# Kernel optimization log

Measured on AMD Instinct MI355X. Metric: run time of the kernel, lower is better.

## Reference

```python
import jax, jax.numpy as jnp
import numpy as np

B, I, H = 8192, 1024, 1024

def setup_inputs() -> dict:
    key = jax.random.key(0)
    ks = jax.random.split(key, 6)
    s_in = 1.0 / np.sqrt(I)
    s_h = 1.0 / np.sqrt(H)
    return {
        "x": jax.random.normal(ks[0], (B, I), jnp.float32),
        "h_prev": jax.random.normal(ks[1], (B, H), jnp.float32),
        "c_prev": jax.random.normal(ks[2], (B, H), jnp.float32),
        "Wx": jax.random.normal(ks[3], (4, H, I), jnp.float32) * s_in,   # gate order: input, forget, cell, output
        "Wh": jax.random.normal(ks[4], (4, H, H), jnp.float32) * s_h,
        "bh": jax.random.normal(ks[5], (4, H), jnp.float32) * s_h,
    }

def reference(x, h_prev, c_prev, Wx, Wh, bh):
    # Fused: 2 batched GEMMs for all 4 gates -> [B, 4, H]
    gates = (jnp.einsum('bi,ghi->bgh', x, Wx)
             + jnp.einsum('bk,ghk->bgh', h_prev, Wh)
             + bh[None, :, :])
    i = jax.nn.sigmoid(gates[:, 0])
    f = jax.nn.sigmoid(gates[:, 1])
    g = jnp.tanh(gates[:, 2])
    o = jax.nn.sigmoid(gates[:, 3])
    c_next = f * c_prev + i * g
    h_next = o * jnp.tanh(c_next)
    return (h_next, c_next)
```

## Files before the change

### kernel.cpp

```cpp
#include <hip/hip_runtime.h>
#include <hip/hip_bf16.h>
#include <stdint.h>

#define B_DIM 8192
#define I_DIM 1024
#define H_DIM 1024
#define KTOT  2048
#define NTILES 32

typedef __attribute__((ext_vector_type(8))) short short8;
typedef __attribute__((ext_vector_type(4))) float f32x4;

static __device__ __forceinline__ short f2b(float f) {
    __bf16 h = (__bf16)f;
    return __builtin_bit_cast(short, h);
}

static __device__ __forceinline__ short8 pack8(float4 a, float4 b) {
    short8 s;
    s[0] = f2b(a.x); s[1] = f2b(a.y); s[2] = f2b(a.z); s[3] = f2b(a.w);
    s[4] = f2b(b.x); s[5] = f2b(b.y); s[6] = f2b(b.z); s[7] = f2b(b.w);
    return s;
}

static __device__ __forceinline__ float sigmoid_f(float x) {
    return 1.0f / (1.0f + __expf(-x));
}

static __device__ __forceinline__ float tanh_fast(float x) {
    x = fminf(fmaxf(x, -15.0f), 15.0f);
    float e = __expf(2.0f * x);
    return (e - 1.0f) / (e + 1.0f);
}

static __device__ __forceinline__ void load_lds16(const void* gptr, void* lptr) {
    __builtin_amdgcn_global_load_lds(
        (const __attribute__((address_space(1))) uint32_t*)gptr,
        (__attribute__((address_space(3))) uint32_t*)lptr, 16, 0, 0);
}

__global__ __launch_bounds__(256) void convert_kernel(
    const float* __restrict__ x, const float* __restrict__ h,
    const float* __restrict__ wx, const float* __restrict__ wh,
    short* __restrict__ Aw, short* __restrict__ Bw)
{
    const int64_t nx = (int64_t)B_DIM * I_DIM / 8;
    const int64_t nw = (int64_t)4 * H_DIM * I_DIM / 8;
    const int64_t total = 2 * nx + 2 * nw;
    for (int64_t g = (int64_t)blockIdx.x * blockDim.x + threadIdx.x; g < total;
         g += (int64_t)gridDim.x * blockDim.x) {
        const float* src;
        short* dst;
        if (g < nx) {
            int64_t r = g >> 7, kc = (g & 127) * 8;
            src = x + g * 8; dst = Aw + r * 2048 + kc;
        } else if (g < 2 * nx) {
            int64_t gg = g - nx;
            int64_t r = gg >> 7, kc = (gg & 127) * 8;
            src = h + gg * 8; dst = Aw + r * 2048 + 1024 + kc;
        } else if (g < 2 * nx + nw) {
            int64_t gg = g - 2 * nx;
            int64_t r = gg >> 7, kc = (gg & 127) * 8;
            src = wx + gg * 8; dst = Bw + r * 2048 + kc;
        } else {
            int64_t gg = g - 2 * nx - nw;
            int64_t r = gg >> 7, kc = (gg & 127) * 8;
            src = wh + gg * 8; dst = Bw + r * 2048 + 1024 + kc;
        }
        float4 v0 = ((const float4*)src)[0];
        float4 v1 = ((const float4*)src)[1];
        *(short8*)dst = pack8(v0, v1);
    }
}


#define AOFF(d, kp, f) ((d) * 16384 + (kp) * 8192 + (f) * 512)
#define BOFF(d, kp, f) (32768 + (d) * 16384 + (kp) * 8192 + (f) * 512)

#define STAGE_A(dn, kh, tkp) \
    load_lds16(aSrc0 + (size_t)(tkp) * 64 + (kh) * 32, &smem[AOFF(dn, kh, 2 * w)]); \
    load_lds16(aSrc1 + (size_t)(tkp) * 64 + (kh) * 32, &smem[AOFF(dn, kh, 2 * w + 1)]);

#define STAGE_B(dn, kh, tkp) \
    load_lds16(bSrc0 + (size_t)(tkp) * 64 + (kh) * 32, &smem[BOFF(dn, kh, 2 * w)]); \
    load_lds16(bSrc1 + (size_t)(tkp) * 64 + (kh) * 32, &smem[BOFF(dn, kh, 2 * w + 1)]);

#define VM4 asm volatile("s_waitcnt vmcnt(4)" ::: "memory");

#define PH(d, kp, mh, AV, BV, STAGE_STMT, EXTRAWAIT) do { \
    _Pragma("unroll") \
    for (int j = 0; j < 4; ++j) \
        BV[j] = *(const short8*)&smem[BOFF(d, kp, wn * 4 + j) + lane * 8]; \
    _Pragma("unroll") \
    for (int i = 0; i < 4; ++i) \
        AV[i] = *(const short8*)&smem[AOFF(d, kp, wm * 8 + (mh) * 4 + i) + lane * 8]; \
    STAGE_STMT \
    __builtin_amdgcn_s_barrier(); \
    __builtin_amdgcn_s_setprio(1); \
    _Pragma("unroll") \
    for (int i = 0; i < 4; ++i) \
        _Pragma("unroll") \
        for (int j = 0; j < 4; ++j) \
            acc[(mh) * 4 + i][j] = __builtin_amdgcn_mfma_f32_16x16x32_bf16( \
                AV[i], BV[j], acc[(mh) * 4 + i][j], 0, 0, 0); \
    __builtin_amdgcn_s_setprio(0); \
    EXTRAWAIT \
    __builtin_amdgcn_s_barrier(); \
} while (0)

#define TILE(d, tn) do { \
    PH(d, 0, 0, avA, bvA, STAGE_A(d ^ 1, 0, tn), ); \
    PH(d, 0, 1, avB, bvB, STAGE_B(d ^ 1, 0, tn), VM4); \
    PH(d, 1, 0, avA, bvA, STAGE_A(d ^ 1, 1, tn), ); \
    PH(d, 1, 1, avB, bvB, STAGE_B(d ^ 1, 1, tn), VM4); \
} while (0)

__global__ __launch_bounds__(512, 2) void lstm_gemm8_kernel(
    const short* __restrict__ Aw, const short* __restrict__ Bw,
    const float* __restrict__ cprev, const float* __restrict__ bh,
    float* __restrict__ out)
{
    extern __shared__ __align__(16) short smem[];

    int bid = blockIdx.x;
    bid = (bid & 7) * 64 + (bid >> 3);
    const int bm = bid >> 4;
    const int bn = bid & 15;
    const int m0 = bm * 256;
    const int h0 = bn * 64;

    const int t    = threadIdx.x;
    const int lane = t & 63;
    const int w    = t >> 6;
    const int wm   = w >> 2;
    const int wn   = w & 3;
    const int lc   = lane & 15;
    const int lk   = lane >> 4;

    const short* aSrc0 = Aw + (size_t)(m0 + (2 * w + 0) * 16 + lc) * 2048 + lk * 8;
    const short* aSrc1 = Aw + (size_t)(m0 + (2 * w + 1) * 16 + lc) * 2048 + lk * 8;
    const int cf0 = 2 * w, cf1 = 2 * w + 1;
    const short* bSrc0 = Bw + (size_t)((cf0 & 3) * 1024 + h0 + ((cf0 >> 2) << 4) + lc) * 2048 + lk * 8;
    const short* bSrc1 = Bw + (size_t)((cf1 & 3) * 1024 + h0 + ((cf1 >> 2) << 4) + lc) * 2048 + lk * 8;

    f32x4 acc[8][4] = {};
    short8 avA[4], avB[4], bvA[4], bvB[4];

    STAGE_A(0, 0, 0)
    STAGE_B(0, 0, 0)
    STAGE_A(0, 1, 0)
    STAGE_B(0, 1, 0)
    asm volatile("s_waitcnt vmcnt(0)" ::: "memory");
    __builtin_amdgcn_s_barrier();

    #pragma unroll 1
    for (int tk2 = 0; tk2 < 16; ++tk2) {
        const int t1  = 2 * tk2 + 1;
        const int tp1 = (t1 + 1 < NTILES) ? t1 + 1 : t1;
        TILE(0, t1);
        TILE(1, tp1);
    }
    asm volatile("s_waitcnt vmcnt(0)" ::: "memory");

    const int rg = lane >> 4;
    const int h  = h0 + wn * 16 + lc;
    const float b_i = bh[0 * H_DIM + h];
    const float b_f = bh[1 * H_DIM + h];
    const float b_g = bh[2 * H_DIM + h];
    const float b_o = bh[3 * H_DIM + h];

    #pragma unroll
    for (int mf = 0; mf < 8; ++mf) {
        #pragma unroll
        for (int r = 0; r < 4; ++r) {
            const int row = m0 + wm * 128 + mf * 16 + rg * 4 + r;
            const float pi = acc[mf][0][r] + b_i;
            const float pf = acc[mf][1][r] + b_f;
            const float pg = acc[mf][2][r] + b_g;
            const float po = acc[mf][3][r] + b_o;
            const float iv = sigmoid_f(pi);
            const float fv = sigmoid_f(pf);
            const float gv = tanh_fast(pg);
            const float ov = sigmoid_f(po);
            const float cp = cprev[(size_t)row * H_DIM + h];
            const float cn = fv * cp + iv * gv;
            const float hn = ov * tanh_fast(cn);
            out[(size_t)row * H_DIM + h] = hn;
            out[(size_t)B_DIM * H_DIM + (size_t)row * H_DIM + h] = cn;
        }
    }
}

static __device__ __forceinline__ int swz(int row, int k) {
    int byte = (row << 7) + (k << 1);
    byte ^= (row & 7) << 4;
    return byte >> 1;
}

__global__ __launch_bounds__(256, 2) void lstm_fallback_kernel(
    const float* __restrict__ x, const float* __restrict__ hprev,
    const float* __restrict__ cprev, const float* __restrict__ Wx,
    const float* __restrict__ Wh, const float* __restrict__ bh,
    float* __restrict__ out)
{
    __shared__ __align__(16) short As[128 * 64];
    __shared__ __align__(16) short Bs[128 * 64];

    int bid = blockIdx.x;
    bid = (bid & 7) * 256 + (bid >> 3);
    const int mt = bid >> 5;
    const int ht = bid & 31;
    const int m0 = mt * 128;
    const int h0 = ht * 32;

    const int t    = threadIdx.x;
    const int lane = t & 63;
    const int w    = t >> 6;
    const int wr   = w >> 1;
    const int wc   = w & 1;

    const int srow = t >> 3;
    const int sk   = (t & 7) * 8;

    f32x4 acc[4][4] = {};

    #pragma unroll 1
    for (int phase = 0; phase < 2; ++phase) {
        const float* __restrict__ Ap = phase ? hprev : x;
        const float* __restrict__ Bp = phase ? Wh : Wx;
        #pragma unroll 1
        for (int kk = 0; kk < 1024; kk += 64) {
            __syncthreads();
            #pragma unroll
            for (int p = 0; p < 4; ++p) {
                const int row = srow + p * 32;
                const float4* src = (const float4*)(Ap + (size_t)(m0 + row) * I_DIM + kk + sk);
                *(short8*)&As[swz(row, sk)] = pack8(src[0], src[1]);
            }
            #pragma unroll
            for (int p = 0; p < 4; ++p) {
                const int n    = srow + p * 32;
                const int gate = (n >> 4) & 3;
                const int hcol = h0 + ((n >> 6) << 4) + (n & 15);
                const float4* src = (const float4*)(Bp + (size_t)((gate << 10) + hcol) * 1024 + kk + sk);
                *(short8*)&Bs[swz(n, sk)] = pack8(src[0], src[1]);
            }
            __syncthreads();
            #pragma unroll
            for (int ks = 0; ks < 2; ++ks) {
                const int kb = ks * 32 + ((lane >> 4) << 3);
                short8 a[4], b[4];
                #pragma unroll
                for (int m = 0; m < 4; ++m)
                    a[m] = *(const short8*)&As[swz(wr * 64 + m * 16 + (lane & 15), kb)];
                #pragma unroll
                for (int j = 0; j < 4; ++j)
                    b[j] = *(const short8*)&Bs[swz(wc * 64 + j * 16 + (lane & 15), kb)];
                #pragma unroll
                for (int m = 0; m < 4; ++m)
                    #pragma unroll
                    for (int j = 0; j < 4; ++j)
                        acc[m][j] = __builtin_amdgcn_mfma_f32_16x16x32_bf16(a[m], b[j], acc[m][j], 0, 0, 0);
            }
        }
    }

    const int cl = lane & 15;
    const int rg = lane >> 4;
    const int h  = h0 + wc * 16 + cl;
    const float b_i = bh[0 * H_DIM + h];
    const float b_f = bh[1 * H_DIM + h];
    const float b_g = bh[2 * H_DIM + h];
    const float b_o = bh[3 * H_DIM + h];

    #pragma unroll
    for (int m = 0; m < 4; ++m) {
        #pragma unroll
        for (int r = 0; r < 4; ++r) {
            const int row = m0 + wr * 64 + m * 16 + rg * 4 + r;
            const float pi = acc[m][0][r] + b_i;
            const float pf = acc[m][1][r] + b_f;
            const float pg = acc[m][2][r] + b_g;
            const float po = acc[m][3][r] + b_o;
            const float iv = sigmoid_f(pi);
            const float fv = sigmoid_f(pf);
            const float gv = tanh_fast(pg);
            const float ov = sigmoid_f(po);
            const float cp = cprev[(size_t)row * H_DIM + h];
            const float cn = fv * cp + iv * gv;
            const float hn = ov * tanh_fast(cn);
            out[(size_t)row * H_DIM + h] = hn;
            out[(size_t)B_DIM * H_DIM + (size_t)row * H_DIM + h] = cn;
        }
    }
}

extern "C" void kernel_launch(void* const* d_in, const int* in_sizes, int n_in,
                              void* d_out, int out_size, void* d_ws, size_t ws_size,
                              hipStream_t stream) {
    const float* x     = (const float*)d_in[0];
    const float* hprev = (const float*)d_in[1];
    const float* cprev = (const float*)d_in[2];
    const float* Wx    = (const float*)d_in[3];
    const float* Wh    = (const float*)d_in[4];
    const float* bh    = (const float*)d_in[5];
    float* out = (float*)d_out;

    const size_t need = ((size_t)B_DIM * 2048 + (size_t)4096 * 2048) * sizeof(short);
    if (ws_size >= need && d_ws != nullptr) {
        (void)hipFuncSetAttribute((const void*)lstm_gemm8_kernel,
                                  hipFuncAttributeMaxDynamicSharedMemorySize, 131072);
        short* Aw = (short*)d_ws;
        short* Bw = Aw + (size_t)B_DIM * 2048;
        hipLaunchKernelGGL(convert_kernel, dim3(2048), dim3(256), 0, stream,
                           x, hprev, Wx, Wh, Aw, Bw);
        hipLaunchKernelGGL(lstm_gemm8_kernel, dim3(512), dim3(512), 131072, stream,
                           Aw, Bw, cprev, bh, out);
    } else {
        hipLaunchKernelGGL(lstm_fallback_kernel, dim3(2048), dim3(256), 0, stream,
                           x, hprev, cprev, Wx, Wh, bh, out);
    }
}
```

Before: 174.7 us.

## Restructure K-tile schedule: one barrier per tile, all prefetches issued upfront

Each K-tile previously ran as four phases with two barriers apiece. It now has a single barrier per tile. All four global-to-LDS prefetches for the next tile are issued at the start, and LDS fragment reads are interleaved with the MFMA groups using an extra A register set. The aim is to cut barrier synchronization overhead and overlap LDS reads with matrix math. The trade-off is higher register pressure from the additional short8 fragments, plus a full vmcnt(0) wait at the end of each tile that may expose global load latency.

```diff
diff --git a/kernel.cpp b/kernel.cpp
--- a/kernel.cpp
+++ b/kernel.cpp
@@ -85,17 +85,17 @@
     load_lds16(bSrc0 + (size_t)(tkp) * 64 + (kh) * 32, &smem[BOFF(dn, kh, 2 * w)]); \
     load_lds16(bSrc1 + (size_t)(tkp) * 64 + (kh) * 32, &smem[BOFF(dn, kh, 2 * w + 1)]);
 
-#define VM4 asm volatile("s_waitcnt vmcnt(4)" ::: "memory");
-
-#define PH(d, kp, mh, AV, BV, STAGE_STMT, EXTRAWAIT) do { \
+#define RD_B(d, kp, BV) { \
     _Pragma("unroll") \
     for (int j = 0; j < 4; ++j) \
-        BV[j] = *(const short8*)&smem[BOFF(d, kp, wn * 4 + j) + lane * 8]; \
+        BV[j] = *(const short8*)&smem[BOFF(d, kp, wn * 4 + j) + lane * 8]; }
+
+#define RD_A(d, kp, mh, AV) { \
     _Pragma("unroll") \
     for (int i = 0; i < 4; ++i) \
-        AV[i] = *(const short8*)&smem[AOFF(d, kp, wm * 8 + (mh) * 4 + i) + lane * 8]; \
-    STAGE_STMT \
-    __builtin_amdgcn_s_barrier(); \
+        AV[i] = *(const short8*)&smem[AOFF(d, kp, wm * 8 + (mh) * 4 + i) + lane * 8]; }
+
+#define MFMA16(mh, AV, BV) { \
     __builtin_amdgcn_s_setprio(1); \
     _Pragma("unroll") \
     for (int i = 0; i < 4; ++i) \
@@ -103,16 +103,25 @@
         for (int j = 0; j < 4; ++j) \
             acc[(mh) * 4 + i][j] = __builtin_amdgcn_mfma_f32_16x16x32_bf16( \
                 AV[i], BV[j], acc[(mh) * 4 + i][j], 0, 0, 0); \
-    __builtin_amdgcn_s_setprio(0); \
-    EXTRAWAIT \
+    __builtin_amdgcn_s_setprio(0); }
+
+#define TILE(d, tn) do { \
+    RD_B(d, 0, bv0) \
+    RD_A(d, 0, 0, av0) \
+    STAGE_A(d ^ 1, 0, tn) \
+    STAGE_B(d ^ 1, 0, tn) \
+    STAGE_A(d ^ 1, 1, tn) \
+    STAGE_B(d ^ 1, 1, tn) \
+    RD_A(d, 0, 1, av1) \
+    MFMA16(0, av0, bv0) \
+    RD_B(d, 1, bv1) \
+    RD_A(d, 1, 0, av2) \
+    MFMA16(1, av1, bv0) \
+    RD_A(d, 1, 1, av0) \
+    MFMA16(0, av2, bv1) \
+    MFMA16(1, av0, bv1) \
+    asm volatile("s_waitcnt vmcnt(0)" ::: "memory"); \
     __builtin_amdgcn_s_barrier(); \
-} while (0)
-
-#define TILE(d, tn) do { \
-    PH(d, 0, 0, avA, bvA, STAGE_A(d ^ 1, 0, tn), ); \
-    PH(d, 0, 1, avB, bvB, STAGE_B(d ^ 1, 0, tn), VM4); \
-    PH(d, 1, 0, avA, bvA, STAGE_A(d ^ 1, 1, tn), ); \
-    PH(d, 1, 1, avB, bvB, STAGE_B(d ^ 1, 1, tn), VM4); \
 } while (0)
 
 __global__ __launch_bounds__(512, 2) void lstm_gemm8_kernel(
@@ -144,7 +153,7 @@
     const short* bSrc1 = Bw + (size_t)((cf1 & 3) * 1024 + h0 + ((cf1 >> 2) << 4) + lc) * 2048 + lk * 8;
 
     f32x4 acc[8][4] = {};
-    short8 avA[4], avB[4], bvA[4], bvB[4];
+    short8 av0[4], av1[4], av2[4], bv0[4], bv1[4];
 
     STAGE_A(0, 0, 0)
     STAGE_B(0, 0, 0)
```

After: 192.2 us. 1.1x slower.

## Pre-tile bf16 operands into MFMA fragment order for contiguous LDS staging

Applied to the files above, without the earlier changes.

The conversion kernel now writes A and B in a fragment-blocked layout: 16-row fragments by K-tile by half, with 64 lanes of 8 bf16 each. Each direct-to-LDS load of a wave therefore reads a contiguous 1 KB chunk instead of 16 rows strided by 4 KB. The weight fragments are also pre-permuted by gate and column block, which simplifies address math in the GEMM. In exchange, the conversion kernel now does strided, scattered reads from the fp32 sources, and its grid is doubled.

```diff
diff --git a/kernel.cpp b/kernel.cpp
--- a/kernel.cpp
+++ b/kernel.cpp
@@ -39,33 +39,45 @@
         (__attribute__((address_space(3))) uint32_t*)lptr, 16, 0, 0);
 }
 
+#define GA_GROUPS (512 * 32 * 2 * 64)
+#define GB_GROUPS (256 * 32 * 2 * 64)
+
 __global__ __launch_bounds__(256) void convert_kernel(
     const float* __restrict__ x, const float* __restrict__ h,
     const float* __restrict__ wx, const float* __restrict__ wh,
     short* __restrict__ Aw, short* __restrict__ Bw)
 {
-    const int64_t nx = (int64_t)B_DIM * I_DIM / 8;
-    const int64_t nw = (int64_t)4 * H_DIM * I_DIM / 8;
-    const int64_t total = 2 * nx + 2 * nw;
+    const int64_t total = (int64_t)GA_GROUPS + GB_GROUPS;
     for (int64_t g = (int64_t)blockIdx.x * blockDim.x + threadIdx.x; g < total;
          g += (int64_t)gridDim.x * blockDim.x) {
         const float* src;
         short* dst;
-        if (g < nx) {
-            int64_t r = g >> 7, kc = (g & 127) * 8;
-            src = x + g * 8; dst = Aw + r * 2048 + kc;
-        } else if (g < 2 * nx) {
-            int64_t gg = g - nx;
-            int64_t r = gg >> 7, kc = (gg & 127) * 8;
-            src = h + gg * 8; dst = Aw + r * 2048 + 1024 + kc;
-        } else if (g < 2 * nx + nw) {
-            int64_t gg = g - 2 * nx;
-            int64_t r = gg >> 7, kc = (gg & 127) * 8;
-            src = wx + gg * 8; dst = Bw + r * 2048 + kc;
+        if (g < GA_GROUPS) {
+            const int lane = (int)(g & 63);
+            const int rest = (int)(g >> 6);
+            const int kh   = rest & 1;
+            const int tk   = (rest >> 1) & 31;
+            const int mfrag = rest >> 6;
+            const int row = (mfrag << 4) + (lane & 15);
+            const int k   = (tk << 6) + (kh << 5) + ((lane >> 4) << 3);
+            src = (k < 1024) ? (x + (size_t)row * 1024 + k)
+                             : (h + (size_t)row * 1024 + (k - 1024));
+            dst = Aw + (size_t)g * 8;
         } else {
-            int64_t gg = g - 2 * nx - nw;
-            int64_t r = gg >> 7, kc = (gg & 127) * 8;
-            src = wh + gg * 8; dst = Bw + r * 2048 + 1024 + kc;
+            const int64_t gb = g - GA_GROUPS;
+            const int lane = (int)(gb & 63);
+            const int rest = (int)(gb >> 6);
+            const int kh   = rest & 1;
+            const int tk   = (rest >> 1) & 31;
+            const int nfrag = rest >> 6;
+            const int cf   = nfrag & 15;
+            const int bn   = nfrag >> 4;
+            const int gate = cf & 3;
+            const int col  = (bn << 6) + ((cf >> 2) << 4) + (lane & 15);
+            const int k    = (tk << 6) + (kh << 5) + ((lane >> 4) << 3);
+            src = (k < 1024) ? (wx + ((size_t)(gate << 10) + col) * 1024 + k)
+                             : (wh + ((size_t)(gate << 10) + col) * 1024 + (k - 1024));
+            dst = Bw + (size_t)gb * 8;
         }
         float4 v0 = ((const float4*)src)[0];
         float4 v1 = ((const float4*)src)[1];
@@ -78,12 +90,12 @@
 #define BOFF(d, kp, f) (32768 + (d) * 16384 + (kp) * 8192 + (f) * 512)
 
 #define STAGE_A(dn, kh, tkp) \
-    load_lds16(aSrc0 + (size_t)(tkp) * 64 + (kh) * 32, &smem[AOFF(dn, kh, 2 * w)]); \
-    load_lds16(aSrc1 + (size_t)(tkp) * 64 + (kh) * 32, &smem[AOFF(dn, kh, 2 * w + 1)]);
+    load_lds16(aSrc0 + (tkp) * 1024 + (kh) * 512, &smem[AOFF(dn, kh, 2 * w)]); \
+    load_lds16(aSrc1 + (tkp) * 1024 + (kh) * 512, &smem[AOFF(dn, kh, 2 * w + 1)]);
 
 #define STAGE_B(dn, kh, tkp) \
-    load_lds16(bSrc0 + (size_t)(tkp) * 64 + (kh) * 32, &smem[BOFF(dn, kh, 2 * w)]); \
-    load_lds16(bSrc1 + (size_t)(tkp) * 64 + (kh) * 32, &smem[BOFF(dn, kh, 2 * w + 1)]);
+    load_lds16(bSrc0 + (tkp) * 1024 + (kh) * 512, &smem[BOFF(dn, kh, 2 * w)]); \
+    load_lds16(bSrc1 + (tkp) * 1024 + (kh) * 512, &smem[BOFF(dn, kh, 2 * w + 1)]);
 
 #define VM4 asm volatile("s_waitcnt vmcnt(4)" ::: "memory");
 
@@ -135,13 +147,11 @@
     const int wm   = w >> 2;
     const int wn   = w & 3;
     const int lc   = lane & 15;
-    const int lk   = lane >> 4;
-
-    const short* aSrc0 = Aw + (size_t)(m0 + (2 * w + 0) * 16 + lc) * 2048 + lk * 8;
-    const short* aSrc1 = Aw + (size_t)(m0 + (2 * w + 1) * 16 + lc) * 2048 + lk * 8;
-    const int cf0 = 2 * w, cf1 = 2 * w + 1;
-    const short* bSrc0 = Bw + (size_t)((cf0 & 3) * 1024 + h0 + ((cf0 >> 2) << 4) + lc) * 2048 + lk * 8;
-    const short* bSrc1 = Bw + (size_t)((cf1 & 3) * 1024 + h0 + ((cf1 >> 2) << 4) + lc) * 2048 + lk * 8;
+
+    const short* aSrc0 = Aw + (size_t)(bm * 16 + 2 * w + 0) * 32768 + lane * 8;
+    const short* aSrc1 = Aw + (size_t)(bm * 16 + 2 * w + 1) * 32768 + lane * 8;
+    const short* bSrc0 = Bw + (size_t)(bn * 16 + 2 * w + 0) * 32768 + lane * 8;
+    const short* bSrc1 = Bw + (size_t)(bn * 16 + 2 * w + 1) * 32768 + lane * 8;
 
     f32x4 acc[8][4] = {};
     short8 avA[4], avB[4], bvA[4], bvB[4];
@@ -311,8 +321,8 @@
         (void)hipFuncSetAttribute((const void*)lstm_gemm8_kernel,
                                   hipFuncAttributeMaxDynamicSharedMemorySize, 131072);
         short* Aw = (short*)d_ws;
-        short* Bw = Aw + (size_t)B_DIM * 2048;
-        hipLaunchKernelGGL(convert_kernel, dim3(2048), dim3(256), 0, stream,
+        short* Bw = Aw + (size_t)512 * 32768;
+        hipLaunchKernelGGL(convert_kernel, dim3(4096), dim3(256), 0, stream,
                            x, hprev, Wx, Wh, Aw, Bw);
         hipLaunchKernelGGL(lstm_gemm8_kernel, dim3(512), dim3(512), 131072, stream,
                            Aw, Bw, cprev, bh, out);
```

After: 154.2 us. 1.13x faster.
